# Kernel optimization log

Measured on AMD Instinct MI355X. Metric: run time of the kernel, lower is better.

Reference implementation:

```python
import jax, jax.numpy as jnp
import numpy as np

N_NODES = 50000
N_EDGES = 800000
IN_DIM = 768
HID = 128
NUM_CLASSES = 6


def setup_inputs() -> dict:
    key = jax.random.key(0)
    ks = jax.random.split(key, 8)
    x = jax.random.normal(ks[0], (N_NODES, IN_DIM), dtype=jnp.float32)
    edge_index = jax.random.randint(ks[1], (2, N_EDGES), 0, N_NODES, dtype=jnp.int64)
    W1 = jax.random.normal(ks[2], (IN_DIM, HID), dtype=jnp.float32) / np.sqrt(IN_DIM)
    b1 = jnp.zeros((HID,), dtype=jnp.float32)
    W2 = jax.random.normal(ks[3], (HID, HID), dtype=jnp.float32) / np.sqrt(HID)
    b2 = jnp.zeros((HID,), dtype=jnp.float32)
    Wi = jax.random.normal(ks[4], (HID, NUM_CLASSES), dtype=jnp.float32) / np.sqrt(HID)
    bi = jnp.zeros((NUM_CLASSES,), dtype=jnp.float32)
    Wl = jax.random.normal(ks[5], (HID, NUM_CLASSES), dtype=jnp.float32) / np.sqrt(HID)
    bl = jnp.zeros((NUM_CLASSES,), dtype=jnp.float32)
    return {"x": x, "edge_index": edge_index, "W1": W1, "b1": b1,
            "W2": W2, "b2": b2, "Wi": Wi, "bi": bi, "Wl": Wl, "bl": bl}


def gcn_conv(x, src, dst, norm, W, b, num_nodes):
    # PyG GCNConv: h = x W; out[i] = sum_{j->i} norm_ji * h[j] + b
    h = x @ W                                   # [N, out_dim]
    msg = h[src] * norm[:, None]                # [E+N, out_dim] gather
    out = jax.ops.segment_sum(msg, dst, num_segments=num_nodes)  # scatter-add
    return out + b


def reference(x, edge_index, W1, b1, W2, b2, Wi, bi, Wl, bl):
    num_nodes = x.shape[0]
    ei = jnp.clip(edge_index, 0, num_nodes - 1)
    # add self-loops (PyG GCNConv default)
    loop = jnp.arange(num_nodes, dtype=ei.dtype)
    src = jnp.concatenate([ei[0], loop])
    dst = jnp.concatenate([ei[1], loop])
    # symmetric degree normalization deg^-1/2 (deg >= 1 due to self-loops)
    deg = jax.ops.segment_sum(jnp.ones_like(dst, dtype=x.dtype), dst,
                              num_segments=num_nodes)
    dinv = jax.lax.rsqrt(jnp.maximum(deg, 1.0))
    norm = dinv[src] * dinv[dst]                # [E+N]

    h = jax.nn.relu(gcn_conv(x, src, dst, norm, W1, b1, num_nodes))
    # dropout is identity at inference (eval mode)
    h = jax.nn.relu(gcn_conv(h, src, dst, norm, W2, b2, num_nodes))
    impact = jax.nn.log_softmax(h @ Wi + bi, axis=1)
    likelihood = jax.nn.log_softmax(h @ Wl + bl, axis=1)
    return (impact, likelihood)
```

## Files before the change

### kernel.cpp

```cpp
#include <hip/hip_runtime.h>
#include <hip/hip_bf16.h>

#define NN 50000
#define NE 800000
#define KD 768
#define HIDD 128
#define NC 6
#define PADW 64
#define OVCAP 262144

typedef __attribute__((ext_vector_type(8))) short bf16x8;
typedef __attribute__((ext_vector_type(4))) float f32x4;

__device__ __forceinline__ ushort f2bf(float f) {
    union { float f; unsigned u; } v; v.f = f;
    unsigned u = v.u + 0x7FFF + ((v.u >> 16) & 1);
    return (ushort)(u >> 16);
}
__device__ __forceinline__ float bf2f(ushort h) {
    union { unsigned u; float f; } v; v.u = ((unsigned)h) << 16;
    return v.f;
}
__device__ __forceinline__ void gll16(const void* g, void* l) {
    __builtin_amdgcn_global_load_lds((const __attribute__((address_space(1))) void*)g,
                                     (__attribute__((address_space(3))) void*)l, 16, 0, 0);
}
__device__ __forceinline__ float dinv_of(int c) {
    return rsqrtf((float)(c + 1));
}


template <int KTOT>
__device__ __forceinline__ void pack_granule(const float* __restrict__ W,
                                             ushort* __restrict__ WTp, int gi) {
    const int KS = KTOT / 64;
    int ci = gi / (KS * 64);
    int rem = gi % (KS * 64);
    int ks = rem >> 6;
    int lane = rem & 63;
    int lr = lane >> 3;
    int lg = (lane & 7) ^ lr;
    int c = ci * 8 + lr;
    ushort tmp[8];
#pragma unroll
    for (int j = 0; j < 8; ++j)
        tmp[j] = f2bf(W[(size_t)(ks * 64 + lg * 8 + j) * HIDD + c]);
    *(bf16x8*)&WTp[(size_t)gi * 8] = *(bf16x8*)tmp;
}


__global__ void pack_zero_kernel(int* __restrict__ cnt,
                                 const float* __restrict__ W1, const float* __restrict__ W2,
                                 ushort* __restrict__ WT1p, ushort* __restrict__ WT2p) {
    const int PB = 56;
    const int G1 = 16 * (KD / 64) * 64;
    const int G2 = 16 * (HIDD / 64) * 64;
    int b = blockIdx.x;
    if (b < PB) {
        int gi = b * 256 + threadIdx.x;
        if (gi < G1) pack_granule<KD>(W1, WT1p, gi);
        else if (gi < G1 + G2) pack_granule<HIDD>(W2, WT2p, gi - G1);
    } else {
        int i = (b - PB) * 256 + threadIdx.x;
        if (i < NN + 64) cnt[i] = 0;
    }
}


__global__ __launch_bounds__(256) void gemm1_fill_kernel(
    const float* __restrict__ A, const ushort* __restrict__ WTp,
    ushort* __restrict__ out, int M,
    const int* __restrict__ ei, int* __restrict__ cnt,
    int* __restrict__ pad_col, int* __restrict__ ov_cnt, int2* __restrict__ ov) {
    const int GB = (NN + 63) / 64;
    __shared__ ushort As[64 * 64];
    __shared__ ushort Bs[128 * 64];
    if (blockIdx.x >= GB) {
        int e = (blockIdx.x - GB) * 256 + threadIdx.x;
        int sidx = ei[e];
        int d = ei[NE + e];
        sidx = min(max(sidx, 0), NN - 1);
        d = min(max(d, 0), NN - 1);
        int pos = atomicAdd(&cnt[d], 1);
        if (pos < PADW) {
            pad_col[(size_t)d * PADW + pos] = sidx;
        } else {
            int op = atomicAdd(ov_cnt, 1);
            if (op < OVCAP) ov[op] = make_int2(d, sidx);
        }
        return;
    }
    const int KS = KD / 64;
    int t = threadIdx.x;
    int lane = t & 63;
    int wid = t >> 6;
    int wr = wid >> 1, wc = wid & 1;
    int row0 = blockIdx.x * 64;
    f32x4 acc[2][4] = {};

    for (int ks = 0; ks < KS; ++ks) {
        int k0 = ks * 64;
#pragma unroll
        for (int it = 0; it < 4; ++it) {
            int r = (t >> 4) + it * 16;
            int k4 = t & 15;
            int gr = min(row0 + r, M - 1);
            float4 v = *(const float4*)&A[(size_t)gr * KD + k0 + k4 * 4];
            ushort4 w;
            w.x = f2bf(v.x); w.y = f2bf(v.y); w.z = f2bf(v.z); w.w = f2bf(v.w);
            int g = k4 >> 1, half = k4 & 1;
            *(ushort4*)&As[r * 64 + ((g ^ (r & 7)) * 8) + half * 4] = w;
        }
#pragma unroll
        for (int it = 0; it < 4; ++it) {
            int ci = wid * 4 + it;
            gll16(&WTp[(size_t)((ci * KS + ks) * 64 + lane) * 8], &Bs[ci * 512]);
        }
        __syncthreads();
#pragma unroll
        for (int h = 0; h < 2; ++h) {
            int q = h * 4 + (lane >> 4);
            bf16x8 a[2];
#pragma unroll
            for (int m = 0; m < 2; ++m) {
                int r = wr * 32 + m * 16 + (lane & 15);
                a[m] = *(const bf16x8*)&As[r * 64 + (q ^ (r & 7)) * 8];
            }
#pragma unroll
            for (int n = 0; n < 4; ++n) {
                int c = wc * 64 + n * 16 + (lane & 15);
                bf16x8 b = *(const bf16x8*)&Bs[c * 64 + (q ^ (c & 7)) * 8];
#pragma unroll
                for (int m = 0; m < 2; ++m)
                    acc[m][n] = __builtin_amdgcn_mfma_f32_16x16x32_bf16(a[m], b, acc[m][n], 0, 0, 0);
            }
        }
        __syncthreads();
    }
#pragma unroll
    for (int m = 0; m < 2; ++m) {
#pragma unroll
        for (int reg = 0; reg < 4; ++reg) {
            int row = row0 + wr * 32 + m * 16 + (lane >> 4) * 4 + reg;
            if (row < M) {
#pragma unroll
                for (int n = 0; n < 4; ++n) {
                    int colg = wc * 64 + n * 16 + (lane & 15);
                    out[(size_t)row * 128 + colg] = f2bf(acc[m][n][reg]);
                }
            }
        }
    }
}


__global__ __launch_bounds__(256) void mfma_gemm2(const ushort* __restrict__ A,
                                                  const ushort* __restrict__ WTp,
                                                  const int* __restrict__ cnt,
                                                  ushort* __restrict__ out, int M) {
    const int KS = HIDD / 64;
    __shared__ ushort As[64 * 64];
    __shared__ ushort Bs[128 * 64];
    int t = threadIdx.x;
    int lane = t & 63;
    int wid = t >> 6;
    int wr = wid >> 1, wc = wid & 1;
    int row0 = blockIdx.x * 64;
    f32x4 acc[2][4] = {};

    int lr = lane >> 3;
    int lg = (lane & 7) ^ lr;

    for (int ks = 0; ks < KS; ++ks) {
        int k0 = ks * 64;
#pragma unroll
        for (int it = 0; it < 2; ++it) {
            int ci2 = wid * 2 + it;
            int r = ci2 * 8 + lr;
            int gr = min(row0 + r, M - 1);
            gll16(&A[(size_t)gr * HIDD + k0 + lg * 8], &As[ci2 * 512]);
        }
#pragma unroll
        for (int it = 0; it < 4; ++it) {
            int ci = wid * 4 + it;
            gll16(&WTp[(size_t)((ci * KS + ks) * 64 + lane) * 8], &Bs[ci * 512]);
        }
        __syncthreads();
#pragma unroll
        for (int h = 0; h < 2; ++h) {
            int q = h * 4 + (lane >> 4);
            bf16x8 a[2];
#pragma unroll
            for (int m = 0; m < 2; ++m) {
                int r = wr * 32 + m * 16 + (lane & 15);
                a[m] = *(const bf16x8*)&As[r * 64 + (q ^ (r & 7)) * 8];
            }
#pragma unroll
            for (int n = 0; n < 4; ++n) {
                int c = wc * 64 + n * 16 + (lane & 15);
                bf16x8 b = *(const bf16x8*)&Bs[c * 64 + (q ^ (c & 7)) * 8];
#pragma unroll
                for (int m = 0; m < 2; ++m)
                    acc[m][n] = __builtin_amdgcn_mfma_f32_16x16x32_bf16(a[m], b, acc[m][n], 0, 0, 0);
            }
        }
        __syncthreads();
    }
#pragma unroll
    for (int m = 0; m < 2; ++m) {
#pragma unroll
        for (int reg = 0; reg < 4; ++reg) {
            int row = row0 + wr * 32 + m * 16 + (lane >> 4) * 4 + reg;
            if (row < M) {
                float d = dinv_of(cnt[row]);
#pragma unroll
                for (int n = 0; n < 4; ++n) {
                    int colg = wc * 64 + n * 16 + (lane & 15);
                    out[(size_t)row * 128 + colg] = f2bf(acc[m][n][reg] * d);
                }
            }
        }
    }
}


__device__ __forceinline__ void acc_edge(float& ax, float& ay, unsigned w) {
    ax += bf2f((ushort)(w & 0xffff));
    ay += bf2f((ushort)(w >> 16));
}

template <int U>
__device__ __forceinline__ int gather_tier_d(const ushort* __restrict__ hs,
                                             const int* __restrict__ cols,
                                             const int* __restrict__ cnt,
                                             int e, int e1, int l, float& ax, float& ay) {
    for (; e + U <= e1; e += U) {
        int j[U];
#pragma unroll
        for (int u = 0; u < U; ++u) j[u] = cols[e + u];
        unsigned w[U];
        float dj[U];
#pragma unroll
        for (int u = 0; u < U; ++u) {
            w[u] = *(const unsigned*)&hs[(size_t)j[u] * 128 + 2 * l];
            dj[u] = dinv_of(cnt[j[u]]);
        }
#pragma unroll
        for (int u = 0; u < U; ++u) {
            ax = fmaf(dj[u], bf2f((ushort)(w[u] & 0xffff)), ax);
            ay = fmaf(dj[u], bf2f((ushort)(w[u] >> 16)), ay);
        }
    }
    return e;
}

template <int U>
__device__ __forceinline__ int gather_tier(const ushort* __restrict__ hs,
                                           const int* __restrict__ cols,
                                           int e, int e1, int l, float& ax, float& ay) {
    for (; e + U <= e1; e += U) {
        unsigned w[U];
#pragma unroll
        for (int u = 0; u < U; ++u)
            w[u] = *(const unsigned*)&hs[(size_t)cols[e + u] * 128 + 2 * l];
#pragma unroll
        for (int u = 0; u < U; ++u) acc_edge(ax, ay, w[u]);
    }
    return e;
}


__global__ void agg1_kernel(const ushort* __restrict__ hs, const int* __restrict__ cnt,
                            const int* __restrict__ pad_col,
                            const float* __restrict__ bias,
                            const int* __restrict__ ov_cnt, const int2* __restrict__ ov,
                            ushort* __restrict__ out) {
    int wv = threadIdx.x >> 6;
    int l = threadIdx.x & 63;
    int i = blockIdx.x * 4 + wv;
    int deg = cnt[i];
    float d = dinv_of(deg);
    unsigned v0 = *(const unsigned*)&hs[(size_t)i * 128 + 2 * l];
    float ax = d * bf2f((ushort)(v0 & 0xffff));
    float ay = d * bf2f((ushort)(v0 >> 16));
    int n = min(deg, PADW);
    const int* cols = pad_col + (size_t)i * PADW;
    int e = 0;
    e = gather_tier_d<16>(hs, cols, cnt, e, n, l, ax, ay);
    e = gather_tier_d<8>(hs, cols, cnt, e, n, l, ax, ay);
    e = gather_tier_d<4>(hs, cols, cnt, e, n, l, ax, ay);
    for (; e < n; ++e) {
        int j = cols[e];
        unsigned w = *(const unsigned*)&hs[(size_t)j * 128 + 2 * l];
        float dj = dinv_of(cnt[j]);
        ax = fmaf(dj, bf2f((ushort)(w & 0xffff)), ax);
        ay = fmaf(dj, bf2f((ushort)(w >> 16)), ay);
    }
    if (deg > PADW) {
        int oc = min(*ov_cnt, OVCAP);
        for (int k = 0; k < oc; ++k) {
            int2 pr = ov[k];
            if (pr.x == i) {
                unsigned w = *(const unsigned*)&hs[(size_t)pr.y * 128 + 2 * l];
                float dj = dinv_of(cnt[pr.y]);
                ax = fmaf(dj, bf2f((ushort)(w & 0xffff)), ax);
                ay = fmaf(dj, bf2f((ushort)(w >> 16)), ay);
            }
        }
    }
    float ox = fmaxf(fmaf(ax, d, bias[2 * l]), 0.f);
    float oy = fmaxf(fmaf(ay, d, bias[2 * l + 1]), 0.f);
    unsigned o = (unsigned)f2bf(ox) | ((unsigned)f2bf(oy) << 16);
    *(unsigned*)&out[(size_t)i * 128 + 2 * l] = o;
}


__global__ void agg2_heads_kernel(const ushort* __restrict__ hs, const int* __restrict__ cnt,
                                  const int* __restrict__ pad_col,
                                  const float* __restrict__ bias,
                                  const int* __restrict__ ov_cnt, const int2* __restrict__ ov,
                                  const float* __restrict__ Wi, const float* __restrict__ bi,
                                  const float* __restrict__ Wl, const float* __restrict__ bl,
                                  float* __restrict__ out) {
    int wv = threadIdx.x >> 6;
    int l = threadIdx.x & 63;
    int i = blockIdx.x * 4 + wv;
    unsigned v0 = *(const unsigned*)&hs[(size_t)i * 128 + 2 * l];
    float ax = bf2f((ushort)(v0 & 0xffff));
    float ay = bf2f((ushort)(v0 >> 16));
    int deg = cnt[i];
    int n = min(deg, PADW);
    const int* cols = pad_col + (size_t)i * PADW;
    int e = 0;
    e = gather_tier<16>(hs, cols, e, n, l, ax, ay);
    e = gather_tier<8>(hs, cols, e, n, l, ax, ay);
    e = gather_tier<4>(hs, cols, e, n, l, ax, ay);
    for (; e < n; ++e)
        acc_edge(ax, ay, *(const unsigned*)&hs[(size_t)cols[e] * 128 + 2 * l]);
    if (deg > PADW) {
        int oc = min(*ov_cnt, OVCAP);
        for (int k = 0; k < oc; ++k) {
            int2 pr = ov[k];
            if (pr.x == i)
                acc_edge(ax, ay, *(const unsigned*)&hs[(size_t)pr.y * 128 + 2 * l]);
        }
    }
    float d = dinv_of(deg);
    float ox = fmaxf(fmaf(ax, d, bias[2 * l]), 0.f);
    float oy = fmaxf(fmaf(ay, d, bias[2 * l + 1]), 0.f);

    float4 u0 = *(const float4*)&Wi[l * 12];
    float4 u1 = *(const float4*)&Wi[l * 12 + 4];
    float4 u2 = *(const float4*)&Wi[l * 12 + 8];
    float pi[6];
    pi[0] = ox * u0.x + oy * u1.z;
    pi[1] = ox * u0.y + oy * u1.w;
    pi[2] = ox * u0.z + oy * u2.x;
    pi[3] = ox * u0.w + oy * u2.y;
    pi[4] = ox * u1.x + oy * u2.z;
    pi[5] = ox * u1.y + oy * u2.w;
    u0 = *(const float4*)&Wl[l * 12];
    u1 = *(const float4*)&Wl[l * 12 + 4];
    u2 = *(const float4*)&Wl[l * 12 + 8];
    float pl[6];
    pl[0] = ox * u0.x + oy * u1.z;
    pl[1] = ox * u0.y + oy * u1.w;
    pl[2] = ox * u0.z + oy * u2.x;
    pl[3] = ox * u0.w + oy * u2.y;
    pl[4] = ox * u1.x + oy * u2.z;
    pl[5] = ox * u1.y + oy * u2.w;
#pragma unroll
    for (int off = 1; off < 64; off <<= 1) {
#pragma unroll
        for (int c = 0; c < 6; ++c) {
            pi[c] += __shfl_xor(pi[c], off);
            pl[c] += __shfl_xor(pl[c], off);
        }
    }
#pragma unroll
    for (int c = 0; c < 6; ++c) {
        pi[c] += bi[c];
        pl[c] += bl[c];
    }
    float mi = fmaxf(fmaxf(fmaxf(pi[0], pi[1]), fmaxf(pi[2], pi[3])), fmaxf(pi[4], pi[5]));
    float ml = fmaxf(fmaxf(fmaxf(pl[0], pl[1]), fmaxf(pl[2], pl[3])), fmaxf(pl[4], pl[5]));
    float si = 0.f, sl = 0.f;
#pragma unroll
    for (int c = 0; c < 6; ++c) {
        si += expf(pi[c] - mi);
        sl += expf(pl[c] - ml);
    }
    float lsi = mi + logf(si), lsl = ml + logf(sl);
#pragma unroll
    for (int c = 0; c < 6; ++c) {
        if (l == c)     out[(size_t)i * NC + c] = pi[c] - lsi;
        if (l == 6 + c) out[(size_t)NN * NC + (size_t)i * NC + c] = pl[c] - lsl;
    }
}

extern "C" void kernel_launch(void* const* d_in, const int* in_sizes, int n_in,
                              void* d_out, int out_size, void* d_ws, size_t ws_size,
                              hipStream_t stream) {
    const float* x  = (const float*)d_in[0];
    const int*   ei = (const int*)d_in[1];
    const float* W1 = (const float*)d_in[2];
    const float* b1 = (const float*)d_in[3];
    const float* W2 = (const float*)d_in[4];
    const float* b2 = (const float*)d_in[5];
    const float* Wi = (const float*)d_in[6];
    const float* bi = (const float*)d_in[7];
    const float* Wl = (const float*)d_in[8];
    const float* bl = (const float*)d_in[9];
    float* out = (float*)d_out;

    uint8_t* p = (uint8_t*)d_ws;
    auto alloc = [&](size_t bytes) {
        void* r = (void*)p;
        p += (bytes + 255) / 256 * 256;
        return r;
    };
    int* cnt      = (int*)alloc((NN + 64) * sizeof(int));
    int* pad_col  = (int*)alloc((size_t)NN * PADW * sizeof(int));
    int2* ov      = (int2*)alloc((size_t)OVCAP * sizeof(int2));
    ushort* WT1p  = (ushort*)alloc((size_t)KD * HIDD * sizeof(ushort));
    ushort* WT2p  = (ushort*)alloc((size_t)HIDD * HIDD * sizeof(ushort));
    ushort* bufA  = (ushort*)alloc((size_t)NN * HIDD * sizeof(ushort));
    ushort* bufB  = (ushort*)alloc((size_t)NN * HIDD * sizeof(ushort));
    int* ov_cnt = cnt + NN;

    const int FB = NE / 256;
    const int PB = 56;
    const int ZB = (NN + 64 + 255) / 256;
    const int GB = (NN + 63) / 64;

    pack_zero_kernel<<<PB + ZB, 256, 0, stream>>>(cnt, W1, W2, WT1p, WT2p);
    gemm1_fill_kernel<<<GB + FB, 256, 0, stream>>>(x, WT1p, bufA, NN,
                                                   ei, cnt, pad_col, ov_cnt, ov);
    agg1_kernel<<<NN / 4, 256, 0, stream>>>(bufA, cnt, pad_col, b1, ov_cnt, ov, bufB);
    mfma_gemm2<<<GB, 256, 0, stream>>>(bufB, WT2p, cnt, bufA, NN);
    agg2_heads_kernel<<<NN / 4, 256, 0, stream>>>(bufA, cnt, pad_col, b2, ov_cnt, ov,
                                                  Wi, bi, Wl, bl, out);
}
```

Baseline: 174.6 us.

## Fuse layer-1 aggregation with layer-2 GEMM and compress padded adjacency to ushort

```diff
diff --git a/kernel.cpp b/kernel.cpp
--- a/kernel.cpp
+++ b/kernel.cpp
@@ -6,7 +6,7 @@
 #define KD 768
 #define HIDD 128
 #define NC 6
-#define PADW 64
+#define PADW 32
 #define OVCAP 262144
 
 typedef __attribute__((ext_vector_type(8))) short bf16x8;
@@ -55,6 +55,7 @@
     const int PB = 56;
     const int G1 = 16 * (KD / 64) * 64;
     const int G2 = 16 * (HIDD / 64) * 64;
+    const int NZ4 = (NN + 64) / 4 + 1;
     int b = blockIdx.x;
     if (b < PB) {
         int gi = b * 256 + threadIdx.x;
@@ -62,7 +63,7 @@
         else if (gi < G1 + G2) pack_granule<HIDD>(W2, WT2p, gi - G1);
     } else {
         int i = (b - PB) * 256 + threadIdx.x;
-        if (i < NN + 64) cnt[i] = 0;
+        if (i < NZ4) *(int4*)&cnt[i * 4] = make_int4(0, 0, 0, 0);
     }
 }
 
@@ -71,22 +72,28 @@
     const float* __restrict__ A, const ushort* __restrict__ WTp,
     ushort* __restrict__ out, int M,
     const int* __restrict__ ei, int* __restrict__ cnt,
-    int* __restrict__ pad_col, int* __restrict__ ov_cnt, int2* __restrict__ ov) {
+    ushort* __restrict__ pad_col, int* __restrict__ ov_cnt, int2* __restrict__ ov) {
     const int GB = (NN + 63) / 64;
     __shared__ ushort As[64 * 64];
     __shared__ ushort Bs[128 * 64];
     if (blockIdx.x >= GB) {
-        int e = (blockIdx.x - GB) * 256 + threadIdx.x;
-        int sidx = ei[e];
-        int d = ei[NE + e];
-        sidx = min(max(sidx, 0), NN - 1);
-        d = min(max(d, 0), NN - 1);
-        int pos = atomicAdd(&cnt[d], 1);
-        if (pos < PADW) {
-            pad_col[(size_t)d * PADW + pos] = sidx;
-        } else {
-            int op = atomicAdd(ov_cnt, 1);
-            if (op < OVCAP) ov[op] = make_int2(d, sidx);
+        int base_e = (blockIdx.x - GB) * 512 + threadIdx.x;
+#pragma unroll
+        for (int rep = 0; rep < 2; ++rep) {
+            int e = base_e + rep * 256;
+            if (e < NE) {
+                int sidx = ei[e];
+                int d = ei[NE + e];
+                sidx = min(max(sidx, 0), NN - 1);
+                d = min(max(d, 0), NN - 1);
+                int pos = atomicAdd(&cnt[d], 1);
+                if (pos < PADW) {
+                    pad_col[(size_t)d * PADW + pos] = (ushort)sidx;
+                } else {
+                    int op = atomicAdd(ov_cnt, 1);
+                    if (op < OVCAP) ov[op] = make_int2(d, sidx);
+                }
+            }
         }
         return;
     }
@@ -154,76 +161,6 @@
 }
 
 
-__global__ __launch_bounds__(256) void mfma_gemm2(const ushort* __restrict__ A,
-                                                  const ushort* __restrict__ WTp,
-                                                  const int* __restrict__ cnt,
-                                                  ushort* __restrict__ out, int M) {
-    const int KS = HIDD / 64;
-    __shared__ ushort As[64 * 64];
-    __shared__ ushort Bs[128 * 64];
-    int t = threadIdx.x;
-    int lane = t & 63;
-    int wid = t >> 6;
-    int wr = wid >> 1, wc = wid & 1;
-    int row0 = blockIdx.x * 64;
-    f32x4 acc[2][4] = {};
-
-    int lr = lane >> 3;
-    int lg = (lane & 7) ^ lr;
-
-    for (int ks = 0; ks < KS; ++ks) {
-        int k0 = ks * 64;
-#pragma unroll
-        for (int it = 0; it < 2; ++it) {
-            int ci2 = wid * 2 + it;
-            int r = ci2 * 8 + lr;
-            int gr = min(row0 + r, M - 1);
-            gll16(&A[(size_t)gr * HIDD + k0 + lg * 8], &As[ci2 * 512]);
-        }
-#pragma unroll
-        for (int it = 0; it < 4; ++it) {
-            int ci = wid * 4 + it;
-            gll16(&WTp[(size_t)((ci * KS + ks) * 64 + lane) * 8], &Bs[ci * 512]);
-        }
-        __syncthreads();
-#pragma unroll
-        for (int h = 0; h < 2; ++h) {
-            int q = h * 4 + (lane >> 4);
-            bf16x8 a[2];
-#pragma unroll
-            for (int m = 0; m < 2; ++m) {
-                int r = wr * 32 + m * 16 + (lane & 15);
-                a[m] = *(const bf16x8*)&As[r * 64 + (q ^ (r & 7)) * 8];
-            }
-#pragma unroll
-            for (int n = 0; n < 4; ++n) {
-                int c = wc * 64 + n * 16 + (lane & 15);
-                bf16x8 b = *(const bf16x8*)&Bs[c * 64 + (q ^ (c & 7)) * 8];
-#pragma unroll
-                for (int m = 0; m < 2; ++m)
-                    acc[m][n] = __builtin_amdgcn_mfma_f32_16x16x32_bf16(a[m], b, acc[m][n], 0, 0, 0);
-            }
-        }
-        __syncthreads();
-    }
-#pragma unroll
-    for (int m = 0; m < 2; ++m) {
-#pragma unroll
-        for (int reg = 0; reg < 4; ++reg) {
-            int row = row0 + wr * 32 + m * 16 + (lane >> 4) * 4 + reg;
-            if (row < M) {
-                float d = dinv_of(cnt[row]);
-#pragma unroll
-                for (int n = 0; n < 4; ++n) {
-                    int colg = wc * 64 + n * 16 + (lane & 15);
-                    out[(size_t)row * 128 + colg] = f2bf(acc[m][n][reg] * d);
-                }
-            }
-        }
-    }
-}
-
-
 __device__ __forceinline__ void acc_edge(float& ax, float& ay, unsigned w) {
     ax += bf2f((ushort)(w & 0xffff));
     ay += bf2f((ushort)(w >> 16));
@@ -231,7 +168,7 @@
 
 template <int U>
 __device__ __forceinline__ int gather_tier_d(const ushort* __restrict__ hs,
-                                             const int* __restrict__ cols,
+                                             const ushort* __restrict__ cols,
                                              const int* __restrict__ cnt,
                                              int e, int e1, int l, float& ax, float& ay) {
     for (; e + U <= e1; e += U) {
@@ -256,7 +193,7 @@
 
 template <int U>
 __device__ __forceinline__ int gather_tier(const ushort* __restrict__ hs,
-                                           const int* __restrict__ cols,
+                                           const ushort* __restrict__ cols,
                                            int e, int e1, int l, float& ax, float& ay) {
     for (; e + U <= e1; e += U) {
         unsigned w[U];
@@ -270,53 +207,85 @@
 }
 
 
-__global__ void agg1_kernel(const ushort* __restrict__ hs, const int* __restrict__ cnt,
-                            const int* __restrict__ pad_col,
-                            const float* __restrict__ bias,
-                            const int* __restrict__ ov_cnt, const int2* __restrict__ ov,
-                            ushort* __restrict__ out) {
-    int wv = threadIdx.x >> 6;
-    int l = threadIdx.x & 63;
-    int i = blockIdx.x * 4 + wv;
-    int deg = cnt[i];
-    float d = dinv_of(deg);
-    unsigned v0 = *(const unsigned*)&hs[(size_t)i * 128 + 2 * l];
-    float ax = d * bf2f((ushort)(v0 & 0xffff));
-    float ay = d * bf2f((ushort)(v0 >> 16));
-    int n = min(deg, PADW);
-    const int* cols = pad_col + (size_t)i * PADW;
-    int e = 0;
-    e = gather_tier_d<16>(hs, cols, cnt, e, n, l, ax, ay);
-    e = gather_tier_d<8>(hs, cols, cnt, e, n, l, ax, ay);
-    e = gather_tier_d<4>(hs, cols, cnt, e, n, l, ax, ay);
-    for (; e < n; ++e) {
-        int j = cols[e];
-        unsigned w = *(const unsigned*)&hs[(size_t)j * 128 + 2 * l];
-        float dj = dinv_of(cnt[j]);
-        ax = fmaf(dj, bf2f((ushort)(w & 0xffff)), ax);
-        ay = fmaf(dj, bf2f((ushort)(w >> 16)), ay);
-    }
-    if (deg > PADW) {
-        int oc = min(*ov_cnt, OVCAP);
-        for (int k = 0; k < oc; ++k) {
-            int2 pr = ov[k];
-            if (pr.x == i) {
-                unsigned w = *(const unsigned*)&hs[(size_t)pr.y * 128 + 2 * l];
-                float dj = dinv_of(cnt[pr.y]);
-                ax = fmaf(dj, bf2f((ushort)(w & 0xffff)), ax);
-                ay = fmaf(dj, bf2f((ushort)(w >> 16)), ay);
+__global__ __launch_bounds__(256) void agg1_gemm2_kernel(
+    const ushort* __restrict__ hs, const int* __restrict__ cnt,
+    const ushort* __restrict__ pad_col, const float* __restrict__ bias,
+    const int* __restrict__ ov_cnt, const int2* __restrict__ ov,
+    const ushort* __restrict__ WT2p, ushort* __restrict__ outp) {
+    __shared__ ushort h1s[16][136];
+    int t = threadIdx.x;
+    int wv = t >> 6;
+    int l = t & 63;
+    for (int k = 0; k < 4; ++k) {
+        int r = wv * 4 + k;
+        int i = blockIdx.x * 16 + r;
+        int deg = cnt[i];
+        float d = dinv_of(deg);
+        unsigned v0 = *(const unsigned*)&hs[(size_t)i * 128 + 2 * l];
+        float ax = d * bf2f((ushort)(v0 & 0xffff));
+        float ay = d * bf2f((ushort)(v0 >> 16));
+        int n = min(deg, PADW);
+        const ushort* cols = pad_col + (size_t)i * PADW;
+        int e = 0;
+        e = gather_tier_d<16>(hs, cols, cnt, e, n, l, ax, ay);
+        e = gather_tier_d<8>(hs, cols, cnt, e, n, l, ax, ay);
+        e = gather_tier_d<4>(hs, cols, cnt, e, n, l, ax, ay);
+        for (; e < n; ++e) {
+            int j = cols[e];
+            unsigned w = *(const unsigned*)&hs[(size_t)j * 128 + 2 * l];
+            float dj = dinv_of(cnt[j]);
+            ax = fmaf(dj, bf2f((ushort)(w & 0xffff)), ax);
+            ay = fmaf(dj, bf2f((ushort)(w >> 16)), ay);
+        }
+        if (deg > PADW) {
+            int oc = min(*ov_cnt, OVCAP);
+            for (int kk = 0; kk < oc; ++kk) {
+                int2 pr = ov[kk];
+                if (pr.x == i) {
+                    unsigned w = *(const unsigned*)&hs[(size_t)pr.y * 128 + 2 * l];
+                    float dj = dinv_of(cnt[pr.y]);
+                    ax = fmaf(dj, bf2f((ushort)(w & 0xffff)), ax);
+                    ay = fmaf(dj, bf2f((ushort)(w >> 16)), ay);
+                }
             }
         }
-    }
-    float ox = fmaxf(fmaf(ax, d, bias[2 * l]), 0.f);
-    float oy = fmaxf(fmaf(ay, d, bias[2 * l + 1]), 0.f);
-    unsigned o = (unsigned)f2bf(ox) | ((unsigned)f2bf(oy) << 16);
-    *(unsigned*)&out[(size_t)i * 128 + 2 * l] = o;
+        float ox = fmaxf(fmaf(ax, d, bias[2 * l]), 0.f);
+        float oy = fmaxf(fmaf(ay, d, bias[2 * l + 1]), 0.f);
+        unsigned o = (unsigned)f2bf(ox) | ((unsigned)f2bf(oy) << 16);
+        *(unsigned*)&h1s[r][2 * l] = o;
+    }
+    __syncthreads();
+    f32x4 acc2[2] = {};
+#pragma unroll
+    for (int ks = 0; ks < 4; ++ks) {
+        int row = l & 15;
+        bf16x8 a = *(const bf16x8*)&h1s[row][ks * 32 + (l >> 4) * 8];
+#pragma unroll
+        for (int n = 0; n < 2; ++n) {
+            int c = wv * 32 + n * 16 + (l & 15);
+            int ci = c >> 3, lr = c & 7;
+            int ks64 = ks >> 1;
+            int q64 = (ks & 1) * 4 + (l >> 4);
+            const bf16x8 b = *(const bf16x8*)&WT2p[(size_t)((ci * 2 + ks64) * 64 + lr * 8 + (q64 ^ lr)) * 8];
+            acc2[n] = __builtin_amdgcn_mfma_f32_16x16x32_bf16(a, b, acc2[n], 0, 0, 0);
+        }
+    }
+#pragma unroll
+    for (int n = 0; n < 2; ++n) {
+        int c = wv * 32 + n * 16 + (l & 15);
+#pragma unroll
+        for (int reg = 0; reg < 4; ++reg) {
+            int r = (l >> 4) * 4 + reg;
+            int node = blockIdx.x * 16 + r;
+            float dd = dinv_of(cnt[node]);
+            outp[(size_t)node * 128 + c] = f2bf(acc2[n][reg] * dd);
+        }
+    }
 }
 
 
 __global__ void agg2_heads_kernel(const ushort* __restrict__ hs, const int* __restrict__ cnt,
-                                  const int* __restrict__ pad_col,
+                                  const ushort* __restrict__ pad_col,
                                   const float* __restrict__ bias,
                                   const int* __restrict__ ov_cnt, const int2* __restrict__ ov,
                                   const float* __restrict__ Wi, const float* __restrict__ bi,
@@ -330,7 +299,7 @@
     float ay = bf2f((ushort)(v0 >> 16));
     int deg = cnt[i];
     int n = min(deg, PADW);
-    const int* cols = pad_col + (size_t)i * PADW;
+    const ushort* cols = pad_col + (size_t)i * PADW;
     int e = 0;
     e = gather_tier<16>(hs, cols, e, n, l, ax, ay);
     e = gather_tier<8>(hs, cols, e, n, l, ax, ay);
@@ -419,25 +388,26 @@
         p += (bytes + 255) / 256 * 256;
         return r;
     };
-    int* cnt      = (int*)alloc((NN + 64) * sizeof(int));
-    int* pad_col  = (int*)alloc((size_t)NN * PADW * sizeof(int));
-    int2* ov      = (int2*)alloc((size_t)OVCAP * sizeof(int2));
-    ushort* WT1p  = (ushort*)alloc((size_t)KD * HIDD * sizeof(ushort));
-    ushort* WT2p  = (ushort*)alloc((size_t)HIDD * HIDD * sizeof(ushort));
-    ushort* bufA  = (ushort*)alloc((size_t)NN * HIDD * sizeof(ushort));
-    ushort* bufB  = (ushort*)alloc((size_t)NN * HIDD * sizeof(ushort));
+    int* cnt        = (int*)alloc((NN + 68) * sizeof(int));
+    ushort* pad_col = (ushort*)alloc((size_t)NN * PADW * sizeof(ushort));
+    int2* ov        = (int2*)alloc((size_t)OVCAP * sizeof(int2));
+    ushort* WT1p    = (ushort*)alloc((size_t)KD * HIDD * sizeof(ushort));
+    ushort* WT2p    = (ushort*)alloc((size_t)HIDD * HIDD * sizeof(ushort));
+    ushort* bufA    = (ushort*)alloc((size_t)NN * HIDD * sizeof(ushort));
+    ushort* bufC    = (ushort*)alloc((size_t)NN * HIDD * sizeof(ushort));
     int* ov_cnt = cnt + NN;
 
-    const int FB = NE / 256;
+    const int FB = (NE + 511) / 512;
     const int PB = 56;
-    const int ZB = (NN + 64 + 255) / 256;
+    const int NZ4 = (NN + 64) / 4 + 1;
+    const int ZB = (NZ4 + 255) / 256;
     const int GB = (NN + 63) / 64;
 
     pack_zero_kernel<<<PB + ZB, 256, 0, stream>>>(cnt, W1, W2, WT1p, WT2p);
     gemm1_fill_kernel<<<GB + FB, 256, 0, stream>>>(x, WT1p, bufA, NN,
                                                    ei, cnt, pad_col, ov_cnt, ov);
-    agg1_kernel<<<NN / 4, 256, 0, stream>>>(bufA, cnt, pad_col, b1, ov_cnt, ov, bufB);
-    mfma_gemm2<<<GB, 256, 0, stream>>>(bufB, WT2p, cnt, bufA, NN);
-    agg2_heads_kernel<<<NN / 4, 256, 0, stream>>>(bufA, cnt, pad_col, b2, ov_cnt, ov,
+    agg1_gemm2_kernel<<<NN / 16, 256, 0, stream>>>(bufA, cnt, pad_col, b1, ov_cnt, ov,
+                                                   WT2p, bufC);
+    agg2_heads_kernel<<<NN / 4, 256, 0, stream>>>(bufC, cnt, pad_col, b2, ov_cnt, ov,
                                                   Wi, bi, Wl, bl, out);
 }
```

New measurement: 171.4 us. About the same (-1.9%).
